# Optimization experiments

Hardware: AMD Instinct MI355X
Metric: run time of the kernel (lower is better)

Reference implementation:

```python
import jax, jax.numpy as jnp
import numpy as np

EMBED = 192
D_INNER = 2 * EMBED          # expand=2
D_STATE = 4                  # low_rank
D_CONV = 4
DT_RANK = (EMBED + 15) // 16 # ceil(192/16) = 12
N_MIX = 2
RANK = 4                     # LowRankProjection rank
B_, H_, W_ = 8, 64, 64


def setup_inputs() -> dict:
    key = jax.random.key(0)
    ks = jax.random.split(key, 16)
    s = lambda *sh: 1.0 / np.sqrt(sh[-1])
    inp = {
        "x": jax.random.normal(ks[0], (B_, EMBED, H_, W_), jnp.float32),
        # stacked per-mixer Mamba params (leading dim N_MIX)
        "in_proj_w": jax.random.normal(ks[1], (N_MIX, 2 * D_INNER, EMBED), jnp.float32) * s(EMBED),
        "conv_w": jax.random.normal(ks[2], (N_MIX, D_INNER, D_CONV), jnp.float32) * s(D_CONV),
        "conv_b": jnp.zeros((N_MIX, D_INNER), jnp.float32),
        "x_proj_w": jax.random.normal(ks[3], (N_MIX, DT_RANK + 2 * D_STATE, D_INNER), jnp.float32) * s(D_INNER),
        "dt_proj_w": jax.random.normal(ks[4], (N_MIX, D_INNER, DT_RANK), jnp.float32) * s(DT_RANK),
        "dt_proj_b": jax.random.uniform(ks[5], (N_MIX, D_INNER), jnp.float32, -4.0, -2.0),
        "A_log": jnp.tile(jnp.log(jnp.arange(1, D_STATE + 1, dtype=jnp.float32))[None, None, :], (N_MIX, D_INNER, 1)),
        "D": jnp.ones((N_MIX, D_INNER), jnp.float32),
        "out_proj_w": jax.random.normal(ks[6], (N_MIX, EMBED, D_INNER), jnp.float32) * s(D_INNER),
        # LowRankProjection
        "U_w": jax.random.normal(ks[7], (RANK, EMBED), jnp.float32) * s(EMBED),
        "V_w": jax.random.normal(ks[8], (EMBED, RANK), jnp.float32) * s(RANK),
        # LayerNorm
        "ln_g": jnp.ones((EMBED,), jnp.float32),
        "ln_b": jnp.zeros((EMBED,), jnp.float32),
    }
    return inp


def _silu(x):
    return x * jax.nn.sigmoid(x)


def _mamba(x, in_proj_w, conv_w, conv_b, x_proj_w, dt_proj_w, dt_proj_b, A_log, D, out_proj_w):
    # x: (B, L, d_model)
    B, L, _ = x.shape
    xz = jnp.einsum("bld,ed->ble", x, in_proj_w)          # (B, L, 2*d_inner)
    xin, z = jnp.split(xz, 2, axis=-1)
    # causal depthwise conv over L
    xt = jnp.transpose(xin, (0, 2, 1))                      # (B, d_inner, L)
    xc = jax.lax.conv_general_dilated(
        xt, conv_w[:, None, :], window_strides=(1,), padding=[(D_CONV - 1, 0)],
        feature_group_count=D_INNER, dimension_numbers=("NCH", "OIH", "NCH"))
    xa = _silu(jnp.transpose(xc + conv_b[None, :, None], (0, 2, 1)))  # (B, L, d_inner)
    x_dbl = jnp.einsum("bld,ed->ble", xa, x_proj_w)         # (B, L, dt_rank+2*d_state)
    dt_lr = x_dbl[..., :DT_RANK]
    Bm = x_dbl[..., DT_RANK:DT_RANK + D_STATE]              # (B, L, d_state)
    Cm = x_dbl[..., DT_RANK + D_STATE:]                     # (B, L, d_state)
    dt = jax.nn.softplus(jnp.einsum("blr,dr->bld", dt_lr, dt_proj_w) + dt_proj_b)  # (B, L, d_inner)
    A = -jnp.exp(A_log)                                     # (d_inner, d_state)
    dA = jnp.exp(dt[..., None] * A)                         # (B, L, d_inner, d_state)
    dBu = dt[..., None] * Bm[:, :, None, :] * xa[..., None]  # (B, L, d_inner, d_state)

    def step(h, inputs):
        dA_i, dBu_i, C_i = inputs                           # (B,d_inner,d_state),(B,d_inner,d_state),(B,d_state)
        h = dA_i * h + dBu_i
        y = jnp.einsum("bds,bs->bd", h, C_i)
        return h, y

    h0 = jnp.zeros((B, D_INNER, D_STATE), x.dtype)
    _, ys = jax.lax.scan(step, h0, (jnp.moveaxis(dA, 1, 0), jnp.moveaxis(dBu, 1, 0), jnp.moveaxis(Cm, 1, 0)))
    y = jnp.moveaxis(ys, 0, 1) + xa * D                     # (B, L, d_inner)
    y = y * _silu(z)
    return jnp.einsum("ble,de->bld", y, out_proj_w)         # (B, L, d_model)


def reference(x, in_proj_w, conv_w, conv_b, x_proj_w, dt_proj_w, dt_proj_b,
              A_log, D, out_proj_w, U_w, V_w, ln_g, ln_b):
    residual = x
    B, C, H, W = x.shape
    h = jnp.transpose(x, (0, 2, 3, 1)).reshape(B, H * W, C)
    for i in range(N_MIX):
        h = _mamba(h, in_proj_w[i], conv_w[i], conv_b[i], x_proj_w[i], dt_proj_w[i],
                   dt_proj_b[i], A_log[i], D[i], out_proj_w[i])
    # low-rank projection
    h = jnp.einsum("blr,dr->bld", jnp.einsum("blc,rc->blr", h, U_w), V_w)
    h = jnp.transpose(h.reshape(B, H, W, C), (0, 3, 1, 2)) + residual
    # LayerNorm over channels
    hc = jnp.transpose(h, (0, 2, 3, 1))
    mu = hc.mean(-1, keepdims=True)
    var = ((hc - mu) ** 2).mean(-1, keepdims=True)
    hc = (hc - mu) * jax.lax.rsqrt(var + 1e-5) * ln_g + ln_b
    return jnp.transpose(hc, (0, 3, 1, 2))
```

## Files before the change

### kernel.cpp

```cpp
#include <hip/hip_runtime.h>
#include <hip/hip_bf16.h>
#include <cstdint>

#define EMBED   192
#define DINNER  384
#define DSTATE  4
#define DCONV   4
#define DTRANK  12
#define NMIX    2
#define RANK    4
#define BB      8
#define LL      4096
#define NBL     (BB*LL)
#define NCHUNK  128
#define CLEN    32
#define RSTR    36

typedef __attribute__((ext_vector_type(8))) short short8;
typedef __attribute__((ext_vector_type(4))) float float4v;

static __device__ __forceinline__ ushort f2b(float f) {
    __hip_bfloat16 h = __float2bfloat16(f);
    return *(ushort*)&h;
}
static __device__ __forceinline__ float b2f(ushort u) {
    __hip_bfloat16 h;
    *(ushort*)&h = u;
    return __bfloat162float(h);
}
static __device__ __forceinline__ float bs2f(short s) {
    ushort u = (ushort)s;
    return b2f(u);
}

#define PREP_N0 294912
#define PREP_N1 147456
#define PREP_N2 24576
#define PREP_N3 24576
#define PREP_N4 3072
__global__ __launch_bounds__(256) void k_prep(const float* __restrict__ in_proj_w,
                                              const float* __restrict__ out_proj_w,
                                              const float* __restrict__ x_proj_w,
                                              const float* __restrict__ dt_proj_w,
                                              const float* __restrict__ conv_w,
                                              ushort* __restrict__ wi,
                                              ushort* __restrict__ wo,
                                              ushort* __restrict__ xpwb,
                                              ushort* __restrict__ dtwpad,
                                              float* __restrict__ cwt) {
    int i = blockIdx.x * 256 + threadIdx.x;
    if (i < PREP_N0) {
        wi[i] = f2b(in_proj_w[i]);
        return;
    }
    i -= PREP_N0;
    if (i < PREP_N1) {
        wo[i] = f2b(out_proj_w[i]);
        return;
    }
    i -= PREP_N1;
    if (i < PREP_N2) {
        int mix = i / (32 * 384);
        int rem = i % (32 * 384);
        int e = rem / 384, k = rem % 384;
        xpwb[i] = (e < 20) ? f2b(x_proj_w[(size_t)mix * 20 * 384 + e * 384 + k]) : (ushort)0;
        return;
    }
    i -= PREP_N2;
    if (i < PREP_N3) {
        int mix = i / (384 * 32);
        int rem = i % (384 * 32);
        int n = rem / 32, r = rem % 32;
        dtwpad[i] = (r < DTRANK) ? f2b(dt_proj_w[(size_t)mix * 384 * DTRANK + n * DTRANK + r])
                                 : (ushort)0;
        return;
    }
    i -= PREP_N3;
    if (i < PREP_N4) {
        int mix = i / (DCONV * DINNER);
        int rem = i % (DCONV * DINNER);
        int k = rem / DINNER, d = rem % DINNER;
        cwt[i] = conv_w[(size_t)mix * DINNER * DCONV + d * DCONV + k];
    }
}

__global__ __launch_bounds__(256) void k_transpose(const float* __restrict__ x,
                                                   ushort* __restrict__ h0b) {
    __shared__ float tile[32][33];
    int b  = blockIdx.z;
    int c0 = blockIdx.y * 32;
    int l0 = blockIdx.x * 32;
    int tx = threadIdx.x;
    int ty = threadIdx.y;
    #pragma unroll
    for (int i = 0; i < 4; i++) {
        int c = c0 + ty + i * 8;
        tile[ty + i * 8][tx] = x[((size_t)b * EMBED + c) * LL + l0 + tx];
    }
    __syncthreads();
    #pragma unroll
    for (int i = 0; i < 4; i++) {
        int l = l0 + ty + i * 8;
        h0b[((size_t)b * LL + l) * EMBED + c0 + tx] = f2b(tile[tx][ty + i * 8]);
    }
}

template<int TN, int WRN, bool SILUZ>
__global__ __launch_bounds__(256) void k_gemm_bf16(const ushort* __restrict__ A, int lda,
                                                   const ushort* __restrict__ Bw, int ldb,
                                                   ushort* __restrict__ Cb, int ldcb,
                                                   int K) {
    constexpr int WRM = 4 / WRN;
    constexpr int WM  = 128 / WRM;
    constexpr int MT  = WM / 16;
    __shared__ ushort As[128][40];
    __shared__ ushort Bs[TN][40];
    int tid  = threadIdx.x;
    int lane = tid & 63;
    int wave = tid >> 6;
    int wmo = (wave / WRN) * WM;
    int wno = (wave % WRN) * 64;
    int m0 = blockIdx.x * 128;
    int n0 = blockIdx.y * TN;

    float4v acc[MT][4];
    #pragma unroll
    for (int i = 0; i < MT; i++)
        #pragma unroll
        for (int j = 0; j < 4; j++)
            acc[i][j] = (float4v){0.f, 0.f, 0.f, 0.f};

    for (int k0 = 0; k0 < K; k0 += 32) {
        #pragma unroll
        for (int i = 0; i < 2; i++) {
            int idx = tid + i * 256;
            int r = idx >> 2, sg = idx & 3;
            *(short8*)&As[r][sg * 8] =
                *(const short8*)(A + (size_t)(m0 + r) * lda + k0 + sg * 8);
        }
        #pragma unroll
        for (int i = 0; i < TN / 64; i++) {
            int idx = tid + i * 256;
            int r = idx >> 2, sg = idx & 3;
            *(short8*)&Bs[r][sg * 8] =
                *(const short8*)(Bw + (size_t)(n0 + r) * ldb + k0 + sg * 8);
        }
        __syncthreads();
        short8 av[MT], bv[4];
        #pragma unroll
        for (int i = 0; i < MT; i++)
            av[i] = *(const short8*)&As[wmo + i * 16 + (lane & 15)][(lane >> 4) * 8];
        #pragma unroll
        for (int j = 0; j < 4; j++)
            bv[j] = *(const short8*)&Bs[wno + j * 16 + (lane & 15)][(lane >> 4) * 8];
        #pragma unroll
        for (int i = 0; i < MT; i++)
            #pragma unroll
            for (int j = 0; j < 4; j++)
                acc[i][j] = __builtin_amdgcn_mfma_f32_16x16x32_bf16(
                    av[i], bv[j], acc[i][j], 0, 0, 0);
        __syncthreads();
    }

    #pragma unroll
    for (int i = 0; i < MT; i++) {
        int rbase = m0 + wmo + i * 16 + (lane >> 4) * 4;
        #pragma unroll
        for (int j = 0; j < 4; j++) {
            int col = n0 + wno + j * 16 + (lane & 15);
            #pragma unroll
            for (int r = 0; r < 4; r++) {
                float v = acc[i][j][r];
                if (SILUZ && col >= DINNER) v = v / (1.f + __expf(-v));
                Cb[(size_t)(rbase + r) * ldcb + col] = f2b(v);
            }
        }
    }
}

__global__ __launch_bounds__(256) void k_conv_silu(const ushort* __restrict__ xz,
                                                   const float* __restrict__ cwt,
                                                   const float* __restrict__ cb,
                                                   ushort* __restrict__ xa) {
    int t   = blockIdx.x * 256 + threadIdx.x;
    int g   = t % 48;
    int blc = t / 48;
    int d0  = g * 8;
    int lc  = blc % (LL / 8);
    int b   = blc / (LL / 8);
    int l0  = lc * 8;

    float wk[4][8], bias[8];
    #pragma unroll
    for (int k = 0; k < 4; k++) {
        float4v wa = *(const float4v*)(cwt + k * DINNER + d0);
        float4v wb = *(const float4v*)(cwt + k * DINNER + d0 + 4);
        #pragma unroll
        for (int j = 0; j < 4; j++) { wk[k][j] = wa[j]; wk[k][j + 4] = wb[j]; }
    }
    {
        float4v ba = *(const float4v*)(cb + d0);
        float4v bb = *(const float4v*)(cb + d0 + 4);
        #pragma unroll
        for (int j = 0; j < 4; j++) { bias[j] = ba[j]; bias[j + 4] = bb[j]; }
    }

    float r0[8] = {}, r1[8] = {}, r2[8] = {};
    const ushort* px = xz + ((size_t)(b * LL + l0)) * 768 + d0;
    if (l0 > 0) {
        short8 v;
        v = *(const short8*)(px - 3 * 768);
        #pragma unroll
        for (int j = 0; j < 8; j++) r0[j] = bs2f(v[j]);
        v = *(const short8*)(px - 2 * 768);
        #pragma unroll
        for (int j = 0; j < 8; j++) r1[j] = bs2f(v[j]);
        v = *(const short8*)(px - 1 * 768);
        #pragma unroll
        for (int j = 0; j < 8; j++) r2[j] = bs2f(v[j]);
    }
    ushort* po = xa + ((size_t)(b * LL + l0)) * DINNER + d0;
    #pragma unroll
    for (int i = 0; i < 8; i++) {
        short8 v = *(const short8*)(px + (size_t)i * 768);
        float cur[8];
        #pragma unroll
        for (int j = 0; j < 8; j++) cur[j] = bs2f(v[j]);
        short8 ov;
        #pragma unroll
        for (int j = 0; j < 8; j++) {
            float a = bias[j] + wk[0][j] * r0[j] + wk[1][j] * r1[j]
                    + wk[2][j] * r2[j] + wk[3][j] * cur[j];
            float sv = a / (1.f + __expf(-a));
            ov[j] = (short)f2b(sv);
        }
        *(short8*)(po + (size_t)i * DINNER) = ov;
        #pragma unroll
        for (int j = 0; j < 8; j++) { r0[j] = r1[j]; r1[j] = r2[j]; r2[j] = cur[j]; }
    }
}

__global__ __launch_bounds__(256) void k_xproj_mfma(const ushort* __restrict__ xa,
                                                    const ushort* __restrict__ xpwb,
                                                    float* __restrict__ xdb32) {
    __shared__ ushort As[128][40];
    __shared__ ushort Bs[32][40];
    int tid  = threadIdx.x;
    int lane = tid & 63;
    int wave = tid >> 6;
    int m0 = blockIdx.x * 128;
    float4v acc[2][2];
    #pragma unroll
    for (int i = 0; i < 2; i++)
        #pragma unroll
        for (int j = 0; j < 2; j++)
            acc[i][j] = (float4v){0.f, 0.f, 0.f, 0.f};
    for (int k0 = 0; k0 < 384; k0 += 32) {
        #pragma unroll
        for (int i = 0; i < 2; i++) {
            int idx = tid + i * 256;
            int r = idx >> 2, sg = idx & 3;
            *(short8*)&As[r][sg * 8] =
                *(const short8*)(xa + (size_t)(m0 + r) * 384 + k0 + sg * 8);
        }
        if (tid < 128) {
            int r = tid >> 2, sg = tid & 3;
            *(short8*)&Bs[r][sg * 8] =
                *(const short8*)(xpwb + (size_t)r * 384 + k0 + sg * 8);
        }
        __syncthreads();
        short8 av[2], bv[2];
        #pragma unroll
        for (int i = 0; i < 2; i++)
            av[i] = *(const short8*)&As[wave * 32 + i * 16 + (lane & 15)][(lane >> 4) * 8];
        #pragma unroll
        for (int j = 0; j < 2; j++)
            bv[j] = *(const short8*)&Bs[j * 16 + (lane & 15)][(lane >> 4) * 8];
        #pragma unroll
        for (int i = 0; i < 2; i++)
            #pragma unroll
            for (int j = 0; j < 2; j++)
                acc[i][j] = __builtin_amdgcn_mfma_f32_16x16x32_bf16(
                    av[i], bv[j], acc[i][j], 0, 0, 0);
        __syncthreads();
    }
    #pragma unroll
    for (int i = 0; i < 2; i++) {
        int rbase = m0 + wave * 32 + i * 16 + (lane >> 4) * 4;
        #pragma unroll
        for (int j = 0; j < 2; j++) {
            int col = j * 16 + (lane & 15);
            #pragma unroll
            for (int r = 0; r < 4; r++)
                xdb32[(size_t)(rbase + r) * 32 + col] = acc[i][j][r];
        }
    }
}

static __device__ __forceinline__ void dt_mfma_tile(const float* __restrict__ rows,
                                                    const ushort* __restrict__ dtwpad,
                                                    const float* __restrict__ dtb,
                                                    ushort* __restrict__ dtS,
                                                    int wave, int lane) {
    int mcol = lane & 15;
    int quad = lane >> 4;
    #pragma unroll
    for (int nt = 0; nt < 4; nt++) {
        int n = wave * 64 + nt * 16 + mcol;
        short8 bv = *(const short8*)(dtwpad + (size_t)n * 32 + quad * 8);
        float bias = dtb[n];
        #pragma unroll
        for (int mt = 0; mt < 2; mt++) {
            float4v a0 = *(const float4v*)&rows[(mt * 16 + mcol) * RSTR + quad * 8];
            float4v a1 = *(const float4v*)&rows[(mt * 16 + mcol) * RSTR + quad * 8 + 4];
            short8 av;
            #pragma unroll
            for (int j = 0; j < 4; j++) {
                av[j]     = (short)f2b(a0[j]);
                av[j + 4] = (short)f2b(a1[j]);
            }
            float4v acc = (float4v){0.f, 0.f, 0.f, 0.f};
            acc = __builtin_amdgcn_mfma_f32_16x16x32_bf16(av, bv, acc, 0, 0, 0);
            #pragma unroll
            for (int r = 0; r < 4; r++) {
                float s = acc[r] + bias;
                float sp = fmaxf(s, 0.f) + __logf(1.f + __expf(-fabsf(s)));
                dtS[(mt * 16 + quad * 4 + r) * DINNER + n] = f2b(sp);
            }
        }
    }
}

static __device__ __forceinline__ bool as_is_harmonic(const float* As) {
    return fabsf(As[1] - 2.f * As[0]) <= 1e-5f * fabsf(As[1]) + 1e-12f
        && fabsf(As[2] - 3.f * As[0]) <= 1e-5f * fabsf(As[2]) + 1e-12f
        && fabsf(As[3] - 4.f * As[0]) <= 1e-5f * fabsf(As[3]) + 1e-12f;
}

__global__ __launch_bounds__(384) void k_scan_local(const ushort* __restrict__ xa,
                                                    const float* __restrict__ xdb32,
                                                    const ushort* __restrict__ dtwpad,
                                                    const float* __restrict__ dtb,
                                                    const float* __restrict__ A_log,
                                                    const float* __restrict__ Dp,
                                                    float* __restrict__ carryT,
                                                    float* __restrict__ carryH,
                                                    uint* __restrict__ dyb) {
    int d     = threadIdx.x;
    int lane  = d & 63;
    int wave  = d >> 6;
    int chunk = blockIdx.x;
    int b     = blockIdx.y;
    __shared__ float rows[CLEN * RSTR];
    __shared__ ushort dtS[CLEN * DINNER];
    size_t rbase = ((size_t)b * LL + (size_t)chunk * CLEN) * 32;
    for (int i = d; i < CLEN * 32; i += 384) {
        int l = i >> 5, e = i & 31;
        rows[l * RSTR + e] = xdb32[rbase + i];
    }
    float As[DSTATE];
    #pragma unroll
    for (int s = 0; s < DSTATE; s++) As[s] = -__expf(A_log[d * DSTATE + s]);
    bool fastA = as_is_harmonic(As);
    float Dd = Dp[d];
    __syncthreads();
    dt_mfma_tile(rows, dtwpad, dtb, dtS, wave, lane);
    __syncthreads();
    float h[DSTATE] = {0.f, 0.f, 0.f, 0.f};
    float T = 0.f;
    size_t mbase = (size_t)b * LL + (size_t)chunk * CLEN;
    for (int l = 0; l < CLEN; l++) {
        ushort dtu = dtS[l * DINNER + d];
        float dtvv = b2f(dtu);
        float xav  = b2f(xa[(mbase + l) * DINNER + d]);
        float du   = dtvv * xav;
        T += dtvv;
        const float* row = &rows[l * RSTR];
        float da[DSTATE];
        if (fastA) {
            float p = __expf(dtvv * As[0]);
            da[0] = p; da[1] = p * p; da[2] = da[1] * p; da[3] = da[2] * p;
        } else {
            #pragma unroll
            for (int s = 0; s < DSTATE; s++) da[s] = __expf(dtvv * As[s]);
        }
        float yv = xav * Dd;
        #pragma unroll
        for (int s = 0; s < DSTATE; s++) {
            h[s] = da[s] * h[s] + du * row[DTRANK + s];
            yv  += h[s] * row[DTRANK + DSTATE + s];
        }
        dyb[(mbase + l) * DINNER + d] = ((uint)dtu << 16) | (uint)f2b(yv);
    }
    size_t cb = ((size_t)chunk * BB + b);
    carryT[cb * 384 + d] = T;
    float4v hv = {h[0], h[1], h[2], h[3]};
    *(float4v*)(carryH + cb * 1536 + d * 4) = hv;
}

__global__ __launch_bounds__(256) void k_scan_combine(const float* __restrict__ carryT,
                                                      const float* __restrict__ carryH,
                                                      const float* __restrict__ A_log,
                                                      float* __restrict__ carryI) {
    int c   = blockIdx.x * 256 + threadIdx.x;
    int b   = c / 1536;
    int rem = c - b * 1536;
    int d   = rem >> 2;
    float As = -__expf(A_log[rem]);
    float hrun = 0.f;
    for (int k = 0; k < NCHUNK; k++) {
        size_t o = (size_t)k * BB + b;
        float T  = carryT[o * 384 + d];
        float Hk = carryH[o * 1536 + rem];
        carryI[o * 1536 + rem] = hrun;
        hrun = __expf(As * T) * hrun + Hk;
    }
}

__global__ __launch_bounds__(384) void k_scan_corr(const uint* __restrict__ dyb,
                                                   const ushort* __restrict__ xz,
                                                   const float* __restrict__ xdb32,
                                                   const float* __restrict__ A_log,
                                                   const float* __restrict__ carryI,
                                                   ushort* __restrict__ y) {
    int d     = threadIdx.x;
    int chunk = blockIdx.x;
    int b     = blockIdx.y;
    __shared__ float Crow[CLEN][DSTATE];
    size_t rbase = ((size_t)b * LL + (size_t)chunk * CLEN) * 32;
    if (d < CLEN * DSTATE) {
        int l = d >> 2, s = d & 3;
        Crow[l][s] = xdb32[rbase + l * 32 + DTRANK + DSTATE + s];
    }
    float As[DSTATE];
    #pragma unroll
    for (int s = 0; s < DSTATE; s++) As[s] = -__expf(A_log[d * DSTATE + s]);
    bool fastA = as_is_harmonic(As);
    float4v hv = *(const float4v*)(carryI + ((size_t)chunk * BB + b) * 1536 + d * 4);
    float hc[DSTATE];
    #pragma unroll
    for (int s = 0; s < DSTATE; s++) hc[s] = hv[s];
    __syncthreads();
    size_t mbase = (size_t)b * LL + (size_t)chunk * CLEN;
    #pragma unroll 4
    for (int l = 0; l < CLEN; l++) {
        size_t m = mbase + l;
        uint dv = dyb[m * DINNER + d];
        float dtvv = b2f((ushort)(dv >> 16));
        float ylv  = b2f((ushort)(dv & 0xffffu));
        float da[DSTATE];
        if (fastA) {
            float p = __expf(dtvv * As[0]);
            da[0] = p; da[1] = p * p; da[2] = da[1] * p; da[3] = da[2] * p;
        } else {
            #pragma unroll
            for (int s = 0; s < DSTATE; s++) da[s] = __expf(dtvv * As[s]);
        }
        float corr = 0.f;
        #pragma unroll
        for (int s = 0; s < DSTATE; s++) {
            hc[s] *= da[s];
            corr  += hc[s] * Crow[l][s];
        }
        float yv = ylv + corr;
        float zs = b2f(xz[m * 768 + DINNER + d]);
        yv *= zs;
        y[m * DINNER + d] = f2b(yv);
    }
}

__global__ __launch_bounds__(256) void k_tail(const ushort* __restrict__ h1b,
                                              const ushort* __restrict__ h0b,
                                              const float* __restrict__ U,
                                              const float* __restrict__ V,
                                              const float* __restrict__ g,
                                              const float* __restrict__ be,
                                              float* __restrict__ out) {
    __shared__ float tile[EMBED * 65];
    int tid  = threadIdx.x;
    int lane = tid & 63;
    int wave = tid >> 6;
    int b  = blockIdx.y;
    int l0 = blockIdx.x * 64;
    for (int t = 0; t < 16; t++) {
        int lloc = wave * 16 + t;
        size_t m = (size_t)b * LL + l0 + lloc;
        float hv[3];
        #pragma unroll
        for (int i = 0; i < 3; i++) hv[i] = b2f(h1b[m * EMBED + lane + 64 * i]);
        float r[RANK];
        #pragma unroll
        for (int j = 0; j < RANK; j++) {
            float p = 0.f;
            #pragma unroll
            for (int i = 0; i < 3; i++) p += hv[i] * U[j * EMBED + lane + 64 * i];
            #pragma unroll
            for (int off = 1; off < 64; off <<= 1) p += __shfl_xor(p, off);
            r[j] = p;
        }
        float u[3], s1 = 0.f, s2 = 0.f;
        #pragma unroll
        for (int i = 0; i < 3; i++) {
            int c = lane + 64 * i;
            float v = r[0] * V[c * 4 + 0] + r[1] * V[c * 4 + 1]
                    + r[2] * V[c * 4 + 2] + r[3] * V[c * 4 + 3];
            u[i] = v + b2f(h0b[m * EMBED + c]);
            s1 += u[i];
            s2 += u[i] * u[i];
        }
        #pragma unroll
        for (int off = 1; off < 64; off <<= 1) {
            s1 += __shfl_xor(s1, off);
            s2 += __shfl_xor(s2, off);
        }
        float mean = s1 * (1.f / EMBED);
        float var  = s2 * (1.f / EMBED) - mean * mean;
        float inv  = rsqrtf(var + 1e-5f);
        #pragma unroll
        for (int i = 0; i < 3; i++) {
            int c = lane + 64 * i;
            tile[c * 65 + lloc] = (u[i] - mean) * inv * g[c] + be[c];
        }
    }
    __syncthreads();
    for (int i = tid; i < EMBED * 64; i += 256) {
        int c = i >> 6, l = i & 63;
        out[((size_t)(b * EMBED + c)) * LL + l0 + l] = tile[c * 65 + l];
    }
}

extern "C" void kernel_launch(void* const* d_in, const int* in_sizes, int n_in,
                              void* d_out, int out_size, void* d_ws, size_t ws_size,
                              hipStream_t stream) {
    const float* x          = (const float*)d_in[0];
    const float* in_proj_w  = (const float*)d_in[1];
    const float* conv_w     = (const float*)d_in[2];
    const float* conv_b     = (const float*)d_in[3];
    const float* x_proj_w   = (const float*)d_in[4];
    const float* dt_proj_w  = (const float*)d_in[5];
    const float* dt_proj_b  = (const float*)d_in[6];
    const float* A_log      = (const float*)d_in[7];
    const float* Dp         = (const float*)d_in[8];
    const float* out_proj_w = (const float*)d_in[9];
    const float* U_w        = (const float*)d_in[10];
    const float* V_w        = (const float*)d_in[11];
    const float* ln_g       = (const float*)d_in[12];
    const float* ln_b       = (const float*)d_in[13];
    float* out = (float*)d_out;

    float* ws    = (float*)d_ws;
    float* xdb32 = ws;
    float* carryT = xdb32 + (size_t)NBL * 32;
    float* carryH = carryT + (size_t)NCHUNK * BB * DINNER;
    float* carryI = carryH + (size_t)NCHUNK * BB * DINNER * DSTATE;
    ushort* xz16   = (ushort*)(carryI + (size_t)NCHUNK * BB * DINNER * DSTATE);
    ushort* xa16   = xz16   + (size_t)NBL * 768;
    ushort* yb     = xa16   + (size_t)NBL * DINNER;
    ushort* h0b    = yb     + (size_t)NBL * DINNER;
    ushort* h1b    = h0b    + (size_t)NBL * EMBED;
    uint*   dyb    = (uint*)(h1b + (size_t)NBL * EMBED);
    ushort* wi     = (ushort*)(dyb + (size_t)NBL * DINNER);
    ushort* wo     = wi     + (size_t)NMIX * 768 * EMBED;
    ushort* xpwb   = wo     + (size_t)NMIX * EMBED * DINNER;
    ushort* dtwpad = xpwb   + (size_t)NMIX * 32 * 384;
    float*  cwt    = (float*)(dtwpad + (size_t)NMIX * 384 * 32);

    k_prep<<<(PREP_N0 + PREP_N1 + PREP_N2 + PREP_N3 + PREP_N4) / 256, 256, 0, stream>>>(
        in_proj_w, out_proj_w, x_proj_w, dt_proj_w, conv_w, wi, wo, xpwb, dtwpad, cwt);

    k_transpose<<<dim3(LL / 32, EMBED / 32, BB), dim3(32, 8), 0, stream>>>(x, h0b);

    const ushort* hinb = h0b;
    for (int mix = 0; mix < NMIX; mix++) {
        const float* Alg  = A_log + (size_t)mix * DINNER * DSTATE;
        const ushort* dtwm = dtwpad + (size_t)mix * 384 * 32;
        const float* dtbm = dt_proj_b + mix * DINNER;

        k_gemm_bf16<128, 2, true><<<dim3(NBL / 128, 768 / 128), 256, 0, stream>>>(
            hinb, EMBED, wi + (size_t)mix * 768 * EMBED, EMBED, xz16, 768, EMBED);
        k_conv_silu<<<(NBL / 8 * 48) / 256, 256, 0, stream>>>(
            xz16, cwt + (size_t)mix * DCONV * DINNER, conv_b + mix * DINNER, xa16);
        k_xproj_mfma<<<NBL / 128, 256, 0, stream>>>(
            xa16, xpwb + (size_t)mix * 32 * 384, xdb32);
        k_scan_local<<<dim3(NCHUNK, BB), 384, 0, stream>>>(
            xa16, xdb32, dtwm, dtbm, Alg, Dp + mix * DINNER, carryT, carryH, dyb);
        k_scan_combine<<<(BB * DINNER * DSTATE) / 256, 256, 0, stream>>>(
            carryT, carryH, Alg, carryI);
        k_scan_corr<<<dim3(NCHUNK, BB), 384, 0, stream>>>(
            dyb, xz16, xdb32, Alg, carryI, yb);
        k_gemm_bf16<64, 1, false><<<dim3(NBL / 128, EMBED / 64), 256, 0, stream>>>(
            yb, DINNER, wo + (size_t)mix * EMBED * DINNER, DINNER, h1b, EMBED, DINNER);
        hinb = h1b;
    }

    k_tail<<<dim3(LL / 64, BB), 256, 0, stream>>>(h1b, h0b, U_w, V_w, ln_g, ln_b, out);
}
```

Baseline: 381.1 us.

## Double-buffer GEMM shared tiles with register prefetch and raise scan unroll factors

The bf16 MFMA GEMM now keeps two LDS buffers for the A and B tiles. The next K-slice is loaded from global memory into registers while MFMAs run on the current buffer, then stored into the other buffer, which leaves one barrier per iteration instead of two. This is meant to hide global load latency behind compute, at the cost of doubled LDS use and extra prefetch registers, which may lower occupancy. Separately, the unroll factors on the scan chunk, combine and correction loops are raised.

Measured after the change: 369.6 us. 3.0% less time.

```diff
diff --git a/kernel.cpp b/kernel.cpp
--- a/kernel.cpp
+++ b/kernel.cpp
@@ -113,11 +113,14 @@
     constexpr int WRM = 4 / WRN;
     constexpr int WM  = 128 / WRM;
     constexpr int MT  = WM / 16;
-    __shared__ ushort As[128][40];
-    __shared__ ushort Bs[TN][40];
+    constexpr int NBU = TN / 64;
+    __shared__ ushort As[2][128][40];
+    __shared__ ushort Bs[2][TN][40];
     int tid  = threadIdx.x;
     int lane = tid & 63;
     int wave = tid >> 6;
+    int mcol = lane & 15;
+    int quad = lane >> 4;
     int wmo = (wave / WRN) * WM;
     int wno = (wave % WRN) * 64;
     int m0 = blockIdx.x * 128;
@@ -130,44 +133,79 @@
         for (int j = 0; j < 4; j++)
             acc[i][j] = (float4v){0.f, 0.f, 0.f, 0.f};
 
+    short8 pa[2], pb[NBU];
+    #pragma unroll
+    for (int i = 0; i < 2; i++) {
+        int idx = tid + i * 256, r = idx >> 2, sg = idx & 3;
+        pa[i] = *(const short8*)(A + (size_t)(m0 + r) * lda + sg * 8);
+    }
+    #pragma unroll
+    for (int i = 0; i < NBU; i++) {
+        int idx = tid + i * 256, r = idx >> 2, sg = idx & 3;
+        pb[i] = *(const short8*)(Bw + (size_t)(n0 + r) * ldb + sg * 8);
+    }
+    #pragma unroll
+    for (int i = 0; i < 2; i++) {
+        int idx = tid + i * 256;
+        *(short8*)&As[0][idx >> 2][(idx & 3) * 8] = pa[i];
+    }
+    #pragma unroll
+    for (int i = 0; i < NBU; i++) {
+        int idx = tid + i * 256;
+        *(short8*)&Bs[0][idx >> 2][(idx & 3) * 8] = pb[i];
+    }
+    __syncthreads();
+
+    int cur = 0;
     for (int k0 = 0; k0 < K; k0 += 32) {
-        #pragma unroll
-        for (int i = 0; i < 2; i++) {
-            int idx = tid + i * 256;
-            int r = idx >> 2, sg = idx & 3;
-            *(short8*)&As[r][sg * 8] =
-                *(const short8*)(A + (size_t)(m0 + r) * lda + k0 + sg * 8);
-        }
-        #pragma unroll
-        for (int i = 0; i < TN / 64; i++) {
-            int idx = tid + i * 256;
-            int r = idx >> 2, sg = idx & 3;
-            *(short8*)&Bs[r][sg * 8] =
-                *(const short8*)(Bw + (size_t)(n0 + r) * ldb + k0 + sg * 8);
-        }
-        __syncthreads();
+        bool more = (k0 + 32) < K;
+        if (more) {
+            #pragma unroll
+            for (int i = 0; i < 2; i++) {
+                int idx = tid + i * 256, r = idx >> 2, sg = idx & 3;
+                pa[i] = *(const short8*)(A + (size_t)(m0 + r) * lda + k0 + 32 + sg * 8);
+            }
+            #pragma unroll
+            for (int i = 0; i < NBU; i++) {
+                int idx = tid + i * 256, r = idx >> 2, sg = idx & 3;
+                pb[i] = *(const short8*)(Bw + (size_t)(n0 + r) * ldb + k0 + 32 + sg * 8);
+            }
+        }
         short8 av[MT], bv[4];
         #pragma unroll
         for (int i = 0; i < MT; i++)
-            av[i] = *(const short8*)&As[wmo + i * 16 + (lane & 15)][(lane >> 4) * 8];
+            av[i] = *(const short8*)&As[cur][wmo + i * 16 + mcol][quad * 8];
         #pragma unroll
         for (int j = 0; j < 4; j++)
-            bv[j] = *(const short8*)&Bs[wno + j * 16 + (lane & 15)][(lane >> 4) * 8];
+            bv[j] = *(const short8*)&Bs[cur][wno + j * 16 + mcol][quad * 8];
         #pragma unroll
         for (int i = 0; i < MT; i++)
             #pragma unroll
             for (int j = 0; j < 4; j++)
                 acc[i][j] = __builtin_amdgcn_mfma_f32_16x16x32_bf16(
                     av[i], bv[j], acc[i][j], 0, 0, 0);
+        if (more) {
+            #pragma unroll
+            for (int i = 0; i < 2; i++) {
+                int idx = tid + i * 256;
+                *(short8*)&As[cur ^ 1][idx >> 2][(idx & 3) * 8] = pa[i];
+            }
+            #pragma unroll
+            for (int i = 0; i < NBU; i++) {
+                int idx = tid + i * 256;
+                *(short8*)&Bs[cur ^ 1][idx >> 2][(idx & 3) * 8] = pb[i];
+            }
+        }
         __syncthreads();
+        cur ^= 1;
     }
 
     #pragma unroll
     for (int i = 0; i < MT; i++) {
-        int rbase = m0 + wmo + i * 16 + (lane >> 4) * 4;
+        int rbase = m0 + wmo + i * 16 + quad * 4;
         #pragma unroll
         for (int j = 0; j < 4; j++) {
-            int col = n0 + wno + j * 16 + (lane & 15);
+            int col = n0 + wno + j * 16 + mcol;
             #pragma unroll
             for (int r = 0; r < 4; r++) {
                 float v = acc[i][j][r];
@@ -369,6 +407,7 @@
     float h[DSTATE] = {0.f, 0.f, 0.f, 0.f};
     float T = 0.f;
     size_t mbase = (size_t)b * LL + (size_t)chunk * CLEN;
+    #pragma unroll 8
     for (int l = 0; l < CLEN; l++) {
         ushort dtu = dtS[l * DINNER + d];
         float dtvv = b2f(dtu);
@@ -408,6 +447,7 @@
     int d   = rem >> 2;
     float As = -__expf(A_log[rem]);
     float hrun = 0.f;
+    #pragma unroll 4
     for (int k = 0; k < NCHUNK; k++) {
         size_t o = (size_t)k * BB + b;
         float T  = carryT[o * 384 + d];
@@ -442,7 +482,7 @@
     for (int s = 0; s < DSTATE; s++) hc[s] = hv[s];
     __syncthreads();
     size_t mbase = (size_t)b * LL + (size_t)chunk * CLEN;
-    #pragma unroll 4
+    #pragma unroll 8
     for (int l = 0; l < CLEN; l++) {
         size_t m = mbase + l;
         uint dv = dyb[m * DINNER + d];
```
